# Optimization experiments

Measured on AMD Instinct MI355X. Metric: run time of the kernel, lower is better.

Reference implementation:

```python
import jax, jax.numpy as jnp
import numpy as np

B, DIM, SIZE, NF = 16, 192, 48, 8
C2 = DIM // 2 + 1            # channel-rfft length (97)
HID = int(0.25 * DIM)        # reweight Mlp hidden (48)
FS = SIZE // 2 + 1           # spatial rfft width (25)
EPS = 1e-5


def setup_inputs() -> dict:
    key = jax.random.key(0)
    ks = jax.random.split(key, 12)
    n = lambda i, shape, s=0.02: jax.random.normal(ks[i], shape, jnp.float32) * s
    return {
        "r": jax.random.normal(ks[0], (B, DIM, SIZE, SIZE), jnp.float32),
        "t": jax.random.normal(ks[1], (B, DIM, SIZE, SIZE), jnp.float32),
        # BatchNorm2d (eval mode, running stats mean=0, var=1): [bn_r; bn_t]
        "bn_g": jnp.ones((2, DIM), jnp.float32),
        "bn_b": jnp.zeros((2, DIM), jnp.float32),
        # conv_r / conv_t 1x1 (with bias)
        "crt_w": n(2, (2, DIM, DIM)),
        "crt_b": jnp.zeros((2, DIM), jnp.float32),
        # StarReLU scale/bias: [act_r, act_t, mlp.act]
        "star_s": jnp.ones((3,), jnp.float32),
        "star_b": jnp.zeros((3,), jnp.float32),
        # reweight Mlp (bias=False)
        "fc1_w": n(3, (HID, DIM)),
        "fc2_w": n(4, (NF * DIM, HID)),
        # complex_weights [size, filter_size, num_filters, 2]
        "cw": n(5, (SIZE, FS, NF, 2)),
        # channel-spectrum enhance nets [rc_a, rc_p, tc_a, tc_p], each conv1x1->lrelu->conv1x1
        "enh_w1": n(6, (4, C2, C2)), "enh_b1": jnp.zeros((4, C2), jnp.float32),
        "enh_w2": n(7, (4, C2, C2)), "enh_b2": jnp.zeros((4, C2), jnp.float32),
        # conv_phase_r / conv_phase_t, each conv1x1->lrelu->conv1x1
        "ph_w1": n(8, (2, DIM, DIM)), "ph_b1": jnp.zeros((2, DIM), jnp.float32),
        "ph_w2": n(9, (2, DIM, DIM)), "ph_b2": jnp.zeros((2, DIM), jnp.float32),
        # DwconvFFN: BN (eval) + depthwise 3x3 (no bias)
        "dwbn_g": jnp.ones((DIM,), jnp.float32),
        "dwbn_b": jnp.zeros((DIM,), jnp.float32),
        "dw_w": n(10, (DIM, 1, 3, 3)),
    }


def _leaky(x):
    return jnp.where(x >= 0, x, 0.1 * x)


def _c1(x, w, b):  # 1x1 conv, NCHW
    return jnp.einsum('bchw,oc->bohw', x, w) + b[None, :, None, None]


def _net(x, w1, b1, w2, b2):  # conv1x1 -> LeakyReLU(0.1) -> conv1x1
    return _c1(_leaky(_c1(x, w1, b1)), w2, b2)


def _star(x, s, b):  # StarReLU: s * relu(x)^2 + b
    return s * jnp.square(jnp.maximum(x, 0.0)) + b


def _bn(x, g, b):  # eval-mode BN with running mean=0, var=1
    return x * (g / jnp.sqrt(1.0 + EPS))[None, :, None, None] + b[None, :, None, None]


def _forward(r, t, bn_g, bn_b, crt_w, crt_b, star_s, star_b, fc1_w, fc2_w, cw,
             enh_w1, enh_b1, enh_w2, enh_b2, ph_w1, ph_b1, ph_w2, ph_b2,
             dwbn_g, dwbn_b, dw_w):
    Bsz, D, H, W = r.shape
    res_r, res_t = r, t
    r = _bn(r, bn_g[0], bn_b[0])
    t = _bn(t, bn_g[1], bn_b[1])
    x = r + t
    # routeing: Mlp(mean over HW) -> [B, NF, D] softmax over filters
    h = _star(x.mean((2, 3)) @ fc1_w.T, star_s[2], star_b[2])
    route = jax.nn.softmax((h @ fc2_w.T).reshape(Bsz, NF, D), axis=1)
    r = _star(_c1(r, crt_w[0], crt_b[0]), star_s[0], star_b[0])
    t = _star(_c1(t, crt_w[1], crt_b[1]), star_s[1], star_b[1])

    def branch(u, ia, ip, iph):
        u_fft = jnp.fft.rfft2(u, axes=(2, 3), norm='ortho')   # [B,D,H,FS]
        a = jnp.abs(u_fft)
        p = jnp.angle(u_fft)
        cf = jnp.fft.rfft(a, axis=1, norm='ortho')            # channel rfft -> [B,C2,H,FS]
        ca, cp = jnp.abs(cf), jnp.angle(cf)
        caE = _net(ca, enh_w1[ia], enh_b1[ia], enh_w2[ia], enh_b2[ia])
        cpE = _net(cp, enh_w1[ip], enh_b1[ip], enh_w2[ip], enh_b2[ip])
        comp = caE * jnp.cos(cpE) + 1j * (caE * jnp.sin(cpE))
        c = jnp.fft.irfft(comp, n=D, axis=1, norm='ortho')    # back to [B,D,H,FS]
        sc = c * a
        pE = _net(p, ph_w1[iph], ph_b1[iph], ph_w2[iph], ph_b2[iph])
        return sc * jnp.cos(pE) + 1j * (sc * jnp.sin(pE))

    rt_s = branch(r, 0, 1, 0) + branch(t, 2, 3, 1)            # [B,D,H,FS] complex
    weight = cw[..., 0] + 1j * cw[..., 1]                     # [H,FS,NF]
    weights = jnp.einsum('bfc,hwf->bchw', route.astype(jnp.complex64), weight)
    rt = jnp.fft.irfft2(rt_s * weights, s=(H, W), axes=(2, 3), norm='ortho')
    out_1 = rt + res_r + res_t
    y = _bn(out_1, dwbn_g, dwbn_b)
    y = jax.lax.conv_general_dilated(
        y, dw_w, (1, 1), 'SAME',
        dimension_numbers=('NCHW', 'OIHW', 'NCHW'), feature_group_count=D)
    return y + out_1


def reference(r, t, bn_g, bn_b, crt_w, crt_b, star_s, star_b, fc1_w, fc2_w, cw,
              enh_w1, enh_b1, enh_w2, enh_b2, ph_w1, ph_b1, ph_w2, ph_b2,
              dwbn_g, dwbn_b, dw_w):
    return _forward(r, t, bn_g, bn_b, crt_w, crt_b, star_s, star_b, fc1_w, fc2_w, cw,
                    enh_w1, enh_b1, enh_w2, enh_b2, ph_w1, ph_b1, ph_w2, ph_b2,
                    dwbn_g, dwbn_b, dw_w)
```

## Files before the change

kernel.cpp:

```cpp
#include <hip/hip_runtime.h>
#include <math.h>

constexpr int B_   = 16;
constexpr int D_   = 192;
constexpr int S_   = 48;
constexpr int NF_  = 8;
constexpr int C2_  = 97;
constexpr int HID_ = 48;
constexpr int FS_  = 25;
constexpr int HW_  = S_ * S_;
constexpr int HWF_ = S_ * FS_;
constexpr float EPS_ = 1e-5f;
constexpr double PI_D = 3.14159265358979323846;

__global__ __launch_bounds__(192) void k_prep(const float* __restrict__ crt_w,
                                              const float* __restrict__ crt_b,
                                              const float* __restrict__ bn_g,
                                              const float* __restrict__ bn_b,
                                              float* __restrict__ Weff,
                                              float* __restrict__ beff)
{
    int io = blockIdx.x;
    int c  = threadIdx.x;
    int i  = io / D_;
    float s  = bn_g[i * D_ + c] * rsqrtf(1.f + EPS_);
    float bb = bn_b[i * D_ + c];
    float w  = crt_w[(size_t)io * D_ + c];
    Weff[(size_t)io * D_ + c] = w * s;
    __shared__ float red[D_];
    red[c] = w * bb;
    __syncthreads();
    if (c == 0) {
        float acc = 0.f;
        for (int j = 0; j < D_; ++j) acc += red[j];
        int o = io % D_;
        beff[io] = crt_b[i * D_ + o] + acc;
    }
}

__global__ __launch_bounds__(256) void k_mean(const float* __restrict__ r,
                                              const float* __restrict__ t,
                                              const float* __restrict__ bn_g,
                                              const float* __restrict__ bn_b,
                                              float* __restrict__ xm)
{
    int bd = blockIdx.x;
    int d  = bd % D_;
    float sr = bn_g[d]      * rsqrtf(1.f + EPS_);
    float st = bn_g[D_ + d] * rsqrtf(1.f + EPS_);
    const float* rp = r + (size_t)bd * HW_;
    const float* tp = t + (size_t)bd * HW_;
    float acc = 0.f;
    for (int i = threadIdx.x; i < HW_; i += 256) acc += rp[i] * sr + tp[i] * st;
    __shared__ float red[256];
    red[threadIdx.x] = acc;
    __syncthreads();
    for (int off = 128; off > 0; off >>= 1) {
        if (threadIdx.x < off) red[threadIdx.x] += red[threadIdx.x + off];
        __syncthreads();
    }
    if (threadIdx.x == 0)
        xm[bd] = red[0] * (1.f / HW_) + bn_b[d] + bn_b[D_ + d];
}

__global__ __launch_bounds__(192) void k_route(const float* __restrict__ xm,
                                               const float* __restrict__ fc1,
                                               const float* __restrict__ fc2,
                                               const float* __restrict__ star_s,
                                               const float* __restrict__ star_b,
                                               float* __restrict__ route)
{
    int b = blockIdx.x;
    int tid = threadIdx.x;
    __shared__ float x[D_];
    __shared__ float h[HID_];
    x[tid] = xm[b * D_ + tid];
    __syncthreads();
    if (tid < HID_) {
        float a = 0.f;
        const float* wp = fc1 + (size_t)tid * D_;
        for (int c = 0; c < D_; ++c) a += x[c] * wp[c];
        float rl = fmaxf(a, 0.f);
        h[tid] = star_s[2] * rl * rl + star_b[2];
    }
    __syncthreads();
    float lg[NF_];
    for (int f = 0; f < NF_; ++f) {
        const float* wp = fc2 + ((size_t)f * D_ + tid) * HID_;
        float a = 0.f;
        for (int j = 0; j < HID_; ++j) a += h[j] * wp[j];
        lg[f] = a;
    }
    float m = lg[0];
    for (int f = 1; f < NF_; ++f) m = fmaxf(m, lg[f]);
    float ssum = 0.f;
    for (int f = 0; f < NF_; ++f) { lg[f] = expf(lg[f] - m); ssum += lg[f]; }
    float inv = 1.f / ssum;
    for (int f = 0; f < NF_; ++f)
        route[((size_t)b * NF_ + f) * D_ + tid] = lg[f] * inv;
}

__global__ __launch_bounds__(256) void k_gemm(const float* __restrict__ in,
                                              const float* __restrict__ W,
                                              const float* __restrict__ bias,
                                              float* __restrict__ outp,
                                              int Cin, int Cout, int HWl, int NB, int act,
                                              const float* __restrict__ ssp,
                                              const float* __restrict__ sbp, int sidx,
                                              long instr, long wstr, long bstr, long ostr,
                                              const float* __restrict__ scp,
                                              float* __restrict__ rre,
                                              float* __restrict__ rim, int addf)
{
    const int z = blockIdx.z;
    in   += (long)z * instr;
    W    += (long)z * wstr;
    bias += (long)z * bstr;
    outp += (long)z * ostr;

    const int n0 = blockIdx.x * 128;
    const int o0 = blockIdx.y * 64;
    const int tid = threadIdx.x;
    const int tx = tid & 15;
    const int ty = tid >> 4;
    __shared__ float As[16][72];
    __shared__ float Bs[16][136];
    float acc[4][8] = {};
    const int Ntot = NB * HWl;

    const int akk = tid & 15, aoo0 = tid >> 4;
    const int nn = tid & 127, kb = tid >> 7;
    const int n = n0 + nn;
    const bool nok = n < Ntot;
    int bidx = 0, hw = 0;
    if (nok) { bidx = n / HWl; hw = n % HWl; }
    const float* bp = in + (size_t)bidx * Cin * HWl + hw;

    for (int k0 = 0; k0 < Cin; k0 += 16) {
        #pragma unroll
        for (int j = 0; j < 4; ++j) {
            int oo = aoo0 + 16 * j;
            int o  = o0 + oo;
            int k  = k0 + akk;
            As[akk][oo] = (o < Cout && k < Cin) ? W[(size_t)o * Cin + k] : 0.f;
        }
        #pragma unroll
        for (int j = 0; j < 8; ++j) {
            int kk = kb * 8 + j;
            int k  = k0 + kk;
            Bs[kk][nn] = (nok && k < Cin) ? bp[(size_t)k * HWl] : 0.f;
        }
        __syncthreads();
        #pragma unroll
        for (int kk = 0; kk < 16; ++kk) {
            float4 av = *reinterpret_cast<const float4*>(&As[kk][ty * 4]);
            float4 b0 = *reinterpret_cast<const float4*>(&Bs[kk][tx * 8]);
            float4 b1 = *reinterpret_cast<const float4*>(&Bs[kk][tx * 8 + 4]);
            float a4[4] = {av.x, av.y, av.z, av.w};
            float b8[8] = {b0.x, b0.y, b0.z, b0.w, b1.x, b1.y, b1.z, b1.w};
            #pragma unroll
            for (int i = 0; i < 4; ++i)
                #pragma unroll
                for (int j = 0; j < 8; ++j)
                    acc[i][j] += a4[i] * b8[j];
        }
        __syncthreads();
    }

    float ss = 0.f, sb = 0.f;
    if (act == 2) { ss = ssp[sidx]; sb = sbp[sidx]; }
    #pragma unroll
    for (int i = 0; i < 4; ++i) {
        int o = o0 + ty * 4 + i;
        if (o >= Cout) continue;
        float bs = bias[o];
        #pragma unroll
        for (int j = 0; j < 8; ++j) {
            int nj = n0 + tx * 8 + j;
            if (nj >= Ntot) continue;
            float v = acc[i][j] + bs;
            int bb = nj / HWl, hh = nj % HWl;
            size_t oi = ((size_t)bb * Cout + o) * HWl + hh;
            if (act == 3) {
                float s = scp[oi];
                float sn, cs; sincosf(v, &sn, &cs);
                float re = s * cs, im = s * sn;
                if (addf) { rre[oi] += re; rim[oi] += im; }
                else      { rre[oi]  = re; rim[oi]  = im; }
            } else {
                if (act == 1)      v = v >= 0.f ? v : 0.1f * v;
                else if (act == 2) { float rl = fmaxf(v, 0.f); v = ss * rl * rl + sb; }
                outp[oi] = v;
            }
        }
    }
}

__global__ __launch_bounds__(256) void k_rfft2(const float* __restrict__ u,
                                               float* __restrict__ A,
                                               float* __restrict__ P)
{
    int bd = blockIdx.x;
    __shared__ float tu[HW_];
    __shared__ float rre[HWF_], rim[HWF_];
    __shared__ float tc[S_], ts[S_];
    int t = threadIdx.x;
    if (t < S_) { double ang = -2.0 * PI_D * (double)t / (double)S_; tc[t] = (float)cos(ang); ts[t] = (float)sin(ang); }
    for (int i = t; i < HW_; i += 256) tu[i] = u[(size_t)bd * HW_ + i];
    __syncthreads();
    for (int i = t; i < HWF_; i += 256) {
        int h = i / FS_, k = i % FS_;
        float ar = 0.f, ai = 0.f;
        int m = 0;
        for (int w = 0; w < S_; ++w) {
            float v = tu[h * S_ + w];
            ar += v * tc[m]; ai += v * ts[m];
            m += k; if (m >= S_) m -= S_;
        }
        rre[i] = ar; rim[i] = ai;
    }
    __syncthreads();
    for (int i = t; i < HWF_; i += 256) {
        int kh = i / FS_, w = i % FS_;
        float ar = 0.f, ai = 0.f;
        int m = 0;
        for (int h = 0; h < S_; ++h) {
            float xr = rre[h * FS_ + w], xi = rim[h * FS_ + w];
            float c = tc[m], s = ts[m];
            ar += xr * c - xi * s;
            ai += xr * s + xi * c;
            m += kh; if (m >= S_) m -= S_;
        }
        ar *= (1.f / 48.f); ai *= (1.f / 48.f);
        A[(size_t)bd * HWF_ + i] = sqrtf(ar * ar + ai * ai);
        P[(size_t)bd * HWF_ + i] = atan2f(ai, ar);
    }
}

__global__ __launch_bounds__(256) void k_chfft(const float* __restrict__ A,
                                               float* __restrict__ CA,
                                               float* __restrict__ CP)
{
    int bh = blockIdx.x;
    int b = bh / S_, h = bh % S_;
    __shared__ float ta[D_ * FS_];
    __shared__ float tc[D_], ts[D_];
    int t = threadIdx.x;
    for (int i = t; i < D_; i += 256) {
        double ang = -2.0 * PI_D * (double)i / (double)D_;
        tc[i] = (float)cos(ang); ts[i] = (float)sin(ang);
    }
    for (int i = t; i < D_ * FS_; i += 256) {
        int d = i / FS_, w = i % FS_;
        ta[i] = A[(((size_t)b * D_ + d) * S_ + h) * FS_ + w];
    }
    __syncthreads();
    const float nrm = rsqrtf((float)D_);
    for (int i = t; i < C2_ * FS_; i += 256) {
        int k = i / FS_, w = i % FS_;
        float ar = 0.f, ai = 0.f;
        int m = 0;
        for (int d = 0; d < D_; ++d) {
            float v = ta[d * FS_ + w];
            ar += v * tc[m]; ai += v * ts[m];
            m += k; if (m >= D_) m -= D_;
        }
        ar *= nrm; ai *= nrm;
        size_t o = (((size_t)b * C2_ + k) * S_ + h) * FS_ + w;
        CA[o] = sqrtf(ar * ar + ai * ai);
        CP[o] = atan2f(ai, ar);
    }
}

__global__ __launch_bounds__(256) void k_chirfft(const float* __restrict__ CAe,
                                                 const float* __restrict__ CPe,
                                                 float* __restrict__ Asc)
{
    int bh = blockIdx.x;
    int b = bh / S_, h = bh % S_;
    __shared__ float Ar[C2_ * FS_], Ai[C2_ * FS_];
    __shared__ float tc[D_], ts[D_];
    int t = threadIdx.x;
    for (int i = t; i < D_; i += 256) {
        double ang = 2.0 * PI_D * (double)i / (double)D_;
        tc[i] = (float)cos(ang); ts[i] = (float)sin(ang);
    }
    for (int i = t; i < C2_ * FS_; i += 256) {
        int k = i / FS_, w = i % FS_;
        size_t o = (((size_t)b * C2_ + k) * S_ + h) * FS_ + w;
        float amp = CAe[o], ph = CPe[o];
        float sn, cs; sincosf(ph, &sn, &cs);
        Ar[i] = amp * cs; Ai[i] = amp * sn;
    }
    __syncthreads();
    const float nrm = rsqrtf((float)D_);
    for (int i = t; i < D_ * FS_; i += 256) {
        int d = i / FS_, w = i % FS_;
        float acc = Ar[w] + ((d & 1) ? -1.f : 1.f) * Ar[(C2_ - 1) * FS_ + w];
        float s2 = 0.f;
        int m = d;
        for (int k = 1; k < C2_ - 1; ++k) {
            s2 += Ar[k * FS_ + w] * tc[m] - Ai[k * FS_ + w] * ts[m];
            m += d; if (m >= D_) m -= D_;
        }
        float c = (acc + 2.f * s2) * nrm;
        size_t o = (((size_t)b * D_ + d) * S_ + h) * FS_ + w;
        Asc[o] = c * Asc[o];
    }
}

__global__ __launch_bounds__(256) void k_final(const float* __restrict__ rre,
                                               const float* __restrict__ rim,
                                               const float* __restrict__ route,
                                               const float* __restrict__ cw,
                                               const float* __restrict__ rin,
                                               const float* __restrict__ tin,
                                               float* __restrict__ out1)
{
    int bd = blockIdx.x;
    int b = bd / D_, d = bd % D_;
    __shared__ float sRe[HWF_], sIm[HWF_];
    __shared__ float cRe[HWF_], cIm[HWF_];
    __shared__ float tc[S_], ts[S_];
    __shared__ float rt[NF_];
    int t = threadIdx.x;
    if (t < S_) { double ang = 2.0 * PI_D * (double)t / (double)S_; tc[t] = (float)cos(ang); ts[t] = (float)sin(ang); }
    if (t < NF_) rt[t] = route[((size_t)b * NF_ + t) * D_ + d];
    __syncthreads();
    for (int i = t; i < HWF_; i += 256) {
        const float* cwp = cw + (size_t)i * NF_ * 2;
        float wr = 0.f, wi = 0.f;
        #pragma unroll
        for (int f = 0; f < NF_; ++f) { wr += rt[f] * cwp[2 * f]; wi += rt[f] * cwp[2 * f + 1]; }
        float xr = rre[(size_t)bd * HWF_ + i], xi = rim[(size_t)bd * HWF_ + i];
        sRe[i] = xr * wr - xi * wi;
        sIm[i] = xr * wi + xi * wr;
    }
    __syncthreads();
    for (int i = t; i < HWF_; i += 256) {
        int hp = i / FS_, w = i % FS_;
        float ar = 0.f, ai = 0.f;
        int m = 0;
        for (int h = 0; h < S_; ++h) {
            float xr = sRe[h * FS_ + w], xi = sIm[h * FS_ + w];
            ar += xr * tc[m] - xi * ts[m];
            ai += xr * ts[m] + xi * tc[m];
            m += hp; if (m >= S_) m -= S_;
        }
        cRe[i] = ar; cIm[i] = ai;
    }
    __syncthreads();
    for (int i = t; i < HW_; i += 256) {
        int hp = i / S_, n = i % S_;
        float acc = cRe[hp * FS_] + ((n & 1) ? -1.f : 1.f) * cRe[hp * FS_ + FS_ - 1];
        float s2 = 0.f;
        int m = n;
        for (int k = 1; k < FS_ - 1; ++k) {
            s2 += cRe[hp * FS_ + k] * tc[m] - cIm[hp * FS_ + k] * ts[m];
            m += n; if (m >= S_) m -= S_;
        }
        float v = (acc + 2.f * s2) * (1.f / 48.f);
        size_t o = (size_t)bd * HW_ + i;
        out1[o] = v + rin[o] + tin[o];
    }
}

__global__ __launch_bounds__(256) void k_dw(const float* __restrict__ out1,
                                            const float* __restrict__ g,
                                            const float* __restrict__ bbn,
                                            const float* __restrict__ wdw,
                                            float* __restrict__ outp)
{
    int bd = blockIdx.x;
    int d = bd % D_;
    __shared__ float tile[HW_];
    int t = threadIdx.x;
    for (int i = t; i < HW_; i += 256) tile[i] = out1[(size_t)bd * HW_ + i];
    float sc = g[d] * rsqrtf(1.f + EPS_);
    float bb = bbn[d];
    float w9[9];
    #pragma unroll
    for (int q = 0; q < 9; ++q) w9[q] = wdw[d * 9 + q];
    __syncthreads();
    for (int i = t; i < HW_; i += 256) {
        int y = i / S_, x = i % S_;
        float acc = 0.f;
        #pragma unroll
        for (int ki = 0; ki < 3; ++ki) {
            int yy = y + ki - 1;
            if (yy < 0 || yy >= S_) continue;
            #pragma unroll
            for (int kj = 0; kj < 3; ++kj) {
                int xx = x + kj - 1;
                if (xx < 0 || xx >= S_) continue;
                acc += w9[ki * 3 + kj] * (tile[yy * S_ + xx] * sc + bb);
            }
        }
        outp[(size_t)bd * HW_ + i] = acc + tile[i];
    }
}

extern "C" void kernel_launch(void* const* d_in, const int* in_sizes, int n_in,
                              void* d_out, int out_size, void* d_ws, size_t ws_size,
                              hipStream_t stream)
{
    (void)in_sizes; (void)n_in; (void)out_size; (void)ws_size;
    const float* r      = (const float*)d_in[0];
    const float* t      = (const float*)d_in[1];
    const float* bn_g   = (const float*)d_in[2];
    const float* bn_b   = (const float*)d_in[3];
    const float* crt_w  = (const float*)d_in[4];
    const float* crt_b  = (const float*)d_in[5];
    const float* star_s = (const float*)d_in[6];
    const float* star_b = (const float*)d_in[7];
    const float* fc1_w  = (const float*)d_in[8];
    const float* fc2_w  = (const float*)d_in[9];
    const float* cw     = (const float*)d_in[10];
    const float* enh_w1 = (const float*)d_in[11];
    const float* enh_b1 = (const float*)d_in[12];
    const float* enh_w2 = (const float*)d_in[13];
    const float* enh_b2 = (const float*)d_in[14];
    const float* ph_w1  = (const float*)d_in[15];
    const float* ph_b1  = (const float*)d_in[16];
    const float* ph_w2  = (const float*)d_in[17];
    const float* ph_b2  = (const float*)d_in[18];
    const float* dwbn_g = (const float*)d_in[19];
    const float* dwbn_b = (const float*)d_in[20];
    const float* dw_w   = (const float*)d_in[21];
    float* out = (float*)d_out;

    const long NDHWF = (long)B_ * D_ * HWF_;
    const long SLOTC = (long)B_ * C2_ * HWF_;

    float* ws = (float*)d_ws;
    size_t off = 0;
    float* UACT = ws + off; off += (size_t)B_ * D_ * HW_;
    float* A_   = ws + off; off += NDHWF;
    float* P_   = ws + off; off += NDHWF;
    float* RRE  = ws + off; off += NDHWF;
    float* RIM  = ws + off; off += NDHWF;
    float* CA2  = ws + off; off += 2 * SLOTC;
    float* XM   = ws + off; off += B_ * D_;
    float* ROUTE= ws + off; off += B_ * NF_ * D_;
    float* WEFF = ws + off; off += 2 * D_ * D_;
    float* BEFF = ws + off; off += 2 * D_;
    float* CH   = UACT;
    float* HT   = UACT;

    k_prep<<<2 * D_, D_, 0, stream>>>(crt_w, crt_b, bn_g, bn_b, WEFF, BEFF);
    k_mean<<<B_ * D_, 256, 0, stream>>>(r, t, bn_g, bn_b, XM);
    k_route<<<B_, 192, 0, stream>>>(XM, fc1_w, fc2_w, star_s, star_b, ROUTE);

    for (int br = 0; br < 2; ++br) {
        const float* u_in = (br == 0) ? r : t;
        const int ia = (br == 0) ? 0 : 2;

        k_gemm<<<dim3(288, 3, 1), 256, 0, stream>>>(u_in, WEFF + (size_t)br * D_ * D_, BEFF + br * D_,
            UACT, D_, D_, HW_, B_, 2, star_s, star_b, br, 0, 0, 0, 0, nullptr, nullptr, nullptr, 0);
        k_rfft2<<<B_ * D_, 256, 0, stream>>>(UACT, A_, P_);
        k_chfft<<<B_ * S_, 256, 0, stream>>>(A_, CA2, CA2 + SLOTC);
        k_gemm<<<dim3(150, 2, 2), 256, 0, stream>>>(CA2, enh_w1 + (size_t)ia * C2_ * C2_, enh_b1 + ia * C2_,
            CH, C2_, C2_, HWF_, B_, 1, nullptr, nullptr, 0,
            SLOTC, (long)C2_ * C2_, C2_, SLOTC, nullptr, nullptr, nullptr, 0);
        k_gemm<<<dim3(150, 2, 2), 256, 0, stream>>>(CH, enh_w2 + (size_t)ia * C2_ * C2_, enh_b2 + ia * C2_,
            CA2, C2_, C2_, HWF_, B_, 0, nullptr, nullptr, 0,
            SLOTC, (long)C2_ * C2_, C2_, SLOTC, nullptr, nullptr, nullptr, 0);
        k_chirfft<<<B_ * S_, 256, 0, stream>>>(CA2, CA2 + SLOTC, A_);
        k_gemm<<<dim3(150, 3, 1), 256, 0, stream>>>(P_, ph_w1 + (size_t)br * D_ * D_, ph_b1 + br * D_,
            HT, D_, D_, HWF_, B_, 1, nullptr, nullptr, 0, 0, 0, 0, 0, nullptr, nullptr, nullptr, 0);
        k_gemm<<<dim3(150, 3, 1), 256, 0, stream>>>(HT, ph_w2 + (size_t)br * D_ * D_, ph_b2 + br * D_,
            P_, D_, D_, HWF_, B_, 3, nullptr, nullptr, 0, 0, 0, 0, 0, A_, RRE, RIM, br);
    }

    k_final<<<B_ * D_, 256, 0, stream>>>(RRE, RIM, ROUTE, cw, r, t, UACT);
    k_dw<<<B_ * D_, 256, 0, stream>>>(UACT, dwbn_g, dwbn_b, dw_w, out);
}
```

Measured before the change: 1.501 ms.

## Recast channel DFT and inverse real DFT as tiled GEMMs with precomputed twiddles

Replaces the per-(b,h) direct channel DFT and inverse-rfft kernels with the shared tiled GEMM, multiplying by precomputed cosine/sine twiddle matrices, plus small elementwise kernels for magnitude/phase and for rebuilding real/imag parts. The aim is to turn the O(D*C2) scalar shared-memory loops into register-tiled matmuls with much better data reuse. In exchange it adds extra global-memory passes (abs/angle and the real/imag build write full tensors) and two extra kernel launches per branch. The inverse GEMM fuses the multiply by the spatial amplitude through a new epilogue mode.

```diff
diff --git a/kernel.cpp b/kernel.cpp
--- a/kernel.cpp
+++ b/kernel.cpp
@@ -10,6 +10,7 @@
 constexpr int FS_  = 25;
 constexpr int HW_  = S_ * S_;
 constexpr int HWF_ = S_ * FS_;
+constexpr int CIN2_ = 2 * C2_;
 constexpr float EPS_ = 1e-5f;
 constexpr double PI_D = 3.14159265358979323846;
 
@@ -36,6 +37,36 @@
         int o = io % D_;
         beff[io] = crt_b[i * D_ + o] + acc;
     }
+}
+
+__global__ __launch_bounds__(192) void k_twidf(float* __restrict__ TWF)
+{
+    int k = blockIdx.x;
+    int d = threadIdx.x;
+    double ang = 2.0 * PI_D * (double)(k * d) / (double)D_;
+    float nrm = rsqrtf((float)D_);
+    TWF[k * D_ + d]              = (float)cos(ang) * nrm;
+    TWF[C2_ * D_ + k * D_ + d]   = (float)(-sin(ang)) * nrm;
+}
+
+__global__ __launch_bounds__(256) void k_twidi(float* __restrict__ TWI)
+{
+    int d = blockIdx.x;
+    int k = threadIdx.x;
+    if (k >= CIN2_) return;
+    float nrm = rsqrtf((float)D_);
+    int j = (k < C2_) ? k : k - C2_;
+    double ang = 2.0 * PI_D * (double)(j * d) / (double)D_;
+    float v;
+    if (k < C2_) {
+        if (j == 0)       v = nrm;
+        else if (j == 96) v = (d & 1) ? -nrm : nrm;
+        else              v = 2.f * (float)cos(ang) * nrm;
+    } else {
+        if (j == 0 || j == 96) v = 0.f;
+        else                   v = -2.f * (float)sin(ang) * nrm;
+    }
+    TWI[d * CIN2_ + k] = v;
 }
 
 __global__ __launch_bounds__(256) void k_mean(const float* __restrict__ r,
@@ -115,7 +146,7 @@
     const int z = blockIdx.z;
     in   += (long)z * instr;
     W    += (long)z * wstr;
-    bias += (long)z * bstr;
+    if (bias) bias += (long)z * bstr;
     outp += (long)z * ostr;
 
     const int n0 = blockIdx.x * 128;
@@ -173,7 +204,7 @@
     for (int i = 0; i < 4; ++i) {
         int o = o0 + ty * 4 + i;
         if (o >= Cout) continue;
-        float bs = bias[o];
+        float bs = bias ? bias[o] : 0.f;
         #pragma unroll
         for (int j = 0; j < 8; ++j) {
             int nj = n0 + tx * 8 + j;
@@ -187,6 +218,8 @@
                 float re = s * cs, im = s * sn;
                 if (addf) { rre[oi] += re; rim[oi] += im; }
                 else      { rre[oi]  = re; rim[oi]  = im; }
+            } else if (act == 4) {
+                outp[oi] = v * scp[oi];
             } else {
                 if (act == 1)      v = v >= 0.f ? v : 0.1f * v;
                 else if (act == 2) { float rl = fmaxf(v, 0.f); v = ss * rl * rl + sb; }
@@ -237,75 +270,27 @@
     }
 }
 
-__global__ __launch_bounds__(256) void k_chfft(const float* __restrict__ A,
-                                               float* __restrict__ CA,
-                                               float* __restrict__ CP)
-{
-    int bh = blockIdx.x;
-    int b = bh / S_, h = bh % S_;
-    __shared__ float ta[D_ * FS_];
-    __shared__ float tc[D_], ts[D_];
-    int t = threadIdx.x;
-    for (int i = t; i < D_; i += 256) {
-        double ang = -2.0 * PI_D * (double)i / (double)D_;
-        tc[i] = (float)cos(ang); ts[i] = (float)sin(ang);
-    }
-    for (int i = t; i < D_ * FS_; i += 256) {
-        int d = i / FS_, w = i % FS_;
-        ta[i] = A[(((size_t)b * D_ + d) * S_ + h) * FS_ + w];
-    }
-    __syncthreads();
-    const float nrm = rsqrtf((float)D_);
-    for (int i = t; i < C2_ * FS_; i += 256) {
-        int k = i / FS_, w = i % FS_;
-        float ar = 0.f, ai = 0.f;
-        int m = 0;
-        for (int d = 0; d < D_; ++d) {
-            float v = ta[d * FS_ + w];
-            ar += v * tc[m]; ai += v * ts[m];
-            m += k; if (m >= D_) m -= D_;
-        }
-        ar *= nrm; ai *= nrm;
-        size_t o = (((size_t)b * C2_ + k) * S_ + h) * FS_ + w;
-        CA[o] = sqrtf(ar * ar + ai * ai);
-        CP[o] = atan2f(ai, ar);
-    }
-}
-
-__global__ __launch_bounds__(256) void k_chirfft(const float* __restrict__ CAe,
-                                                 const float* __restrict__ CPe,
-                                                 float* __restrict__ Asc)
-{
-    int bh = blockIdx.x;
-    int b = bh / S_, h = bh % S_;
-    __shared__ float Ar[C2_ * FS_], Ai[C2_ * FS_];
-    __shared__ float tc[D_], ts[D_];
-    int t = threadIdx.x;
-    for (int i = t; i < D_; i += 256) {
-        double ang = 2.0 * PI_D * (double)i / (double)D_;
-        tc[i] = (float)cos(ang); ts[i] = (float)sin(ang);
-    }
-    for (int i = t; i < C2_ * FS_; i += 256) {
-        int k = i / FS_, w = i % FS_;
-        size_t o = (((size_t)b * C2_ + k) * S_ + h) * FS_ + w;
-        float amp = CAe[o], ph = CPe[o];
+__global__ __launch_bounds__(256) void k_absang(float* __restrict__ CF, long slot)
+{
+    for (long i = (long)blockIdx.x * 256 + threadIdx.x; i < slot; i += (long)gridDim.x * 256) {
+        float re = CF[i], im = CF[slot + i];
+        CF[i]        = sqrtf(re * re + im * im);
+        CF[slot + i] = atan2f(im, re);
+    }
+}
+
+__global__ __launch_bounds__(256) void k_buildri(const float* __restrict__ CF,
+                                                 float* __restrict__ RI, long slot)
+{
+    const long row = (long)C2_ * HWF_;
+    const long brow = (long)CIN2_ * HWF_;
+    for (long i = (long)blockIdx.x * 256 + threadIdx.x; i < slot; i += (long)gridDim.x * 256) {
+        long b = i / row;
+        long r = i % row;
+        float amp = CF[i], ph = CF[slot + i];
         float sn, cs; sincosf(ph, &sn, &cs);
-        Ar[i] = amp * cs; Ai[i] = amp * sn;
-    }
-    __syncthreads();
-    const float nrm = rsqrtf((float)D_);
-    for (int i = t; i < D_ * FS_; i += 256) {
-        int d = i / FS_, w = i % FS_;
-        float acc = Ar[w] + ((d & 1) ? -1.f : 1.f) * Ar[(C2_ - 1) * FS_ + w];
-        float s2 = 0.f;
-        int m = d;
-        for (int k = 1; k < C2_ - 1; ++k) {
-            s2 += Ar[k * FS_ + w] * tc[m] - Ai[k * FS_ + w] * ts[m];
-            m += d; if (m >= D_) m -= D_;
-        }
-        float c = (acc + 2.f * s2) * nrm;
-        size_t o = (((size_t)b * D_ + d) * S_ + h) * FS_ + w;
-        Asc[o] = c * Asc[o];
+        RI[b * brow + r]                    = amp * cs;
+        RI[b * brow + (long)C2_ * HWF_ + r] = amp * sn;
     }
 }
 
@@ -444,10 +429,15 @@
     float* ROUTE= ws + off; off += B_ * NF_ * D_;
     float* WEFF = ws + off; off += 2 * D_ * D_;
     float* BEFF = ws + off; off += 2 * D_;
+    float* TWF  = ws + off; off += 2 * C2_ * D_;
+    float* TWI  = ws + off; off += (size_t)D_ * CIN2_;
     float* CH   = UACT;
+    float* RI   = UACT;
     float* HT   = UACT;
 
     k_prep<<<2 * D_, D_, 0, stream>>>(crt_w, crt_b, bn_g, bn_b, WEFF, BEFF);
+    k_twidf<<<C2_, D_, 0, stream>>>(TWF);
+    k_twidi<<<D_, 256, 0, stream>>>(TWI);
     k_mean<<<B_ * D_, 256, 0, stream>>>(r, t, bn_g, bn_b, XM);
     k_route<<<B_, 192, 0, stream>>>(XM, fc1_w, fc2_w, star_s, star_b, ROUTE);
 
@@ -458,14 +448,20 @@
         k_gemm<<<dim3(288, 3, 1), 256, 0, stream>>>(u_in, WEFF + (size_t)br * D_ * D_, BEFF + br * D_,
             UACT, D_, D_, HW_, B_, 2, star_s, star_b, br, 0, 0, 0, 0, nullptr, nullptr, nullptr, 0);
         k_rfft2<<<B_ * D_, 256, 0, stream>>>(UACT, A_, P_);
-        k_chfft<<<B_ * S_, 256, 0, stream>>>(A_, CA2, CA2 + SLOTC);
+        k_gemm<<<dim3(150, 2, 2), 256, 0, stream>>>(A_, TWF, nullptr,
+            CA2, D_, C2_, HWF_, B_, 0, nullptr, nullptr, 0,
+            0, (long)C2_ * D_, 0, SLOTC, nullptr, nullptr, nullptr, 0);
+        k_absang<<<1024, 256, 0, stream>>>(CA2, SLOTC);
         k_gemm<<<dim3(150, 2, 2), 256, 0, stream>>>(CA2, enh_w1 + (size_t)ia * C2_ * C2_, enh_b1 + ia * C2_,
             CH, C2_, C2_, HWF_, B_, 1, nullptr, nullptr, 0,
             SLOTC, (long)C2_ * C2_, C2_, SLOTC, nullptr, nullptr, nullptr, 0);
         k_gemm<<<dim3(150, 2, 2), 256, 0, stream>>>(CH, enh_w2 + (size_t)ia * C2_ * C2_, enh_b2 + ia * C2_,
             CA2, C2_, C2_, HWF_, B_, 0, nullptr, nullptr, 0,
             SLOTC, (long)C2_ * C2_, C2_, SLOTC, nullptr, nullptr, nullptr, 0);
-        k_chirfft<<<B_ * S_, 256, 0, stream>>>(CA2, CA2 + SLOTC, A_);
+        k_buildri<<<1024, 256, 0, stream>>>(CA2, RI, SLOTC);
+        k_gemm<<<dim3(150, 3, 1), 256, 0, stream>>>(RI, TWI, nullptr,
+            A_, CIN2_, D_, HWF_, B_, 4, nullptr, nullptr, 0,
+            0, 0, 0, 0, A_, nullptr, nullptr, 0);
         k_gemm<<<dim3(150, 3, 1), 256, 0, stream>>>(P_, ph_w1 + (size_t)br * D_ * D_, ph_b1 + br * D_,
             HT, D_, D_, HWF_, B_, 1, nullptr, nullptr, 0, 0, 0, 0, 0, nullptr, nullptr, nullptr, 0);
         k_gemm<<<dim3(150, 3, 1), 256, 0, stream>>>(HT, ph_w2 + (size_t)br * D_ * D_, ph_b2 + br * D_,
```

Measured after the change: 1.443 ms. 1.04x faster.
